# Kernel optimization log

Hardware: AMD Instinct MI355X
Metric: run time of the kernel (lower is better)

Reference implementation:

```python
import jax, jax.numpy as jnp
import numpy as np

B, T, A, C = 8, 256, 2, 128
R, H, OUT = 128, 128, 256  # readin_dim, session_embed_size, out_count


def _uni(k, shape, fan_in):
    # matches torch kaiming_uniform_(a=sqrt(5)) / nn.Linear default: U(-1/sqrt(fan_in), 1/sqrt(fan_in))
    b = 1.0 / np.sqrt(fan_in)
    return jax.random.uniform(k, shape, jnp.float32, -b, b)


def setup_inputs() -> dict:
    key = jax.random.key(0)
    ks = jax.random.split(key, 16)
    return {
        "state_in": jax.random.normal(ks[0], (B, T, A, C), jnp.float32),
        "session": jax.random.normal(ks[1], (B, H), jnp.float32),
        "subject": jax.random.normal(ks[2], (B, H), jnp.float32),
        "array": jax.random.normal(ks[3], (B, A, H), jnp.float32),
        "query": jax.random.normal(ks[4], (R,), jnp.float32),
        "pos_embeds": _uni(ks[5], (C, R), R),
        # key_project: Linear(R+H, R) -> GELU -> Linear(R, R); weights stored [in, out]
        "kW1": _uni(ks[6], (R + H, R), R + H), "kb1": _uni(ks[7], (R,), R + H),
        "kW2": _uni(ks[8], (R, R), R), "kb2": _uni(ks[9], (R,), R),
        # value_project: Linear(1+R+H, R) -> GELU -> Linear(R, OUT)
        # concat order in forward is [pos_embed (R), session (H), state_in (1)]
        "vW1": _uni(ks[10], (R + H + 1, R), R + H + 1), "vb1": _uni(ks[11], (R,), R + H + 1),
        "vW2": _uni(ks[12], (R, OUT), R), "vb2": _uni(ks[13], (OUT,), R),
    }


def reference(state_in, session, subject, array, query, pos_embeds,
              kW1, kb1, kW2, kb2, vW1, vb1, vW2, vb2):
    r = pos_embeds.shape[-1]
    h = session.shape[-1]
    scale = jnp.sqrt(jnp.asarray(r, state_in.dtype))
    # keys: cat([pos (c,r) expand b, session (b,h) expand c]) -> MLP. Decompose the
    # first Linear over the concat blocks (same math, no expanded concat buffer).
    kh = (pos_embeds @ kW1[:r])[None, :, :] + (session @ kW1[r:])[:, None, :] + kb1  # [b,c,r]
    keys = jax.nn.gelu(kh, approximate=False) @ kW2 + kb2                           # [b,c,r]
    # values: cat([pos, session, state_in]) over (b,t,a,c) -> MLP, decomposed likewise
    vh = ((pos_embeds @ vW1[:r])[None, None, None, :, :]
          + (session @ vW1[r:r + h])[:, None, None, None, :]
          + state_in[..., None] * vW1[r + h]
          + vb1)                                                                     # [b,t,a,c,r]
    values = jax.nn.gelu(vh, approximate=False) @ vW2 + vb2                          # [b,t,a,c,out]
    scores = jnp.einsum('bcr,r->bc', keys, query) / scale
    w = jax.nn.softmax(scores, axis=-1)                                              # [b,c]
    return jnp.einsum('bc,btach->btah', w, values)                                   # [b,t,a,out]
```

## Files before the change

### kernel.cpp

```cpp
#include <hip/hip_runtime.h>
#include <math.h>

#define B_ 8
#define T_ 256
#define A_ 2
#define C_ 128
#define R_ 128
#define H_ 128
#define OUT_ 256

#define WS_PCK 0
#define WS_PCV 16384
#define WS_PSK 32768
#define WS_PSV 33792
#define WS_QK  34816
#define WS_W   34944
#define WS_TOTAL 35968

__device__ __forceinline__ float gelu_fast(float x) {
    const float ax = fabsf(x);
    float q = fmaf(ax, 0.019527f, 0.000343654f);
    q = fmaf(q, ax, 0.1151945f);
    q = fmaf(q, ax, 0.19685217f);
    q = fmaf(q, ax, 1.0f);
    const float r  = __builtin_amdgcn_rcpf(q);
    const float r2 = r * r;
    const float r4 = r2 * r2;
    return fmaf(-0.5f * ax, r4, fmaxf(x, 0.0f));
}

__global__ __launch_bounds__(256) void prep_kernel(
    const float* __restrict__ session,
    const float* __restrict__ query,
    const float* __restrict__ pos,
    const float* __restrict__ kW1,
    const float* __restrict__ kb1,
    const float* __restrict__ kW2,
    const float* __restrict__ vW1,
    const float* __restrict__ vb1,
    float* __restrict__ ws)
{
    const int g = blockIdx.x * 256 + threadIdx.x;
    if (g < 16384) {
        const int c = g >> 7, r = g & 127;
        float acc = 0.0f;
        #pragma unroll 16
        for (int k = 0; k < R_; ++k)
            acc += pos[c * R_ + k] * kW1[k * R_ + r];
        ws[WS_PCK + g] = acc;
    } else if (g < 32768) {
        const int e = g - 16384;
        const int c = e >> 7, r = e & 127;
        float acc = 0.0f;
        #pragma unroll 16
        for (int k = 0; k < R_; ++k)
            acc += pos[c * R_ + k] * vW1[k * R_ + r];
        ws[WS_PCV + e] = acc;
    } else if (g < 33792) {
        const int e = g - 32768;
        const int b = e >> 7, r = e & 127;
        float acc = kb1[r];
        #pragma unroll 16
        for (int k = 0; k < H_; ++k)
            acc += session[b * H_ + k] * kW1[(R_ + k) * R_ + r];
        ws[WS_PSK + e] = acc;
    } else if (g < 34816) {
        const int e = g - 33792;
        const int b = e >> 7, r = e & 127;
        float acc = vb1[r];
        #pragma unroll 16
        for (int k = 0; k < H_; ++k)
            acc += session[b * H_ + k] * vW1[(R_ + k) * R_ + r];
        ws[WS_PSV + e] = acc;
    } else if (g < 34944) {
        const int r = g - 34816;
        float acc = 0.0f;
        #pragma unroll 16
        for (int j = 0; j < R_; ++j)
            acc += kW2[r * R_ + j] * query[j];
        ws[WS_QK + r] = acc;
    }
}

__global__ __launch_bounds__(512) void score_softmax_kernel(float* __restrict__ ws)
{
    __shared__ float pskL[R_];
    __shared__ float qkL[R_];
    __shared__ float part[4][C_];
    __shared__ float sc[C_];
    __shared__ float red[C_];

    const int b   = blockIdx.x;
    const int tid = threadIdx.x;
    const int q   = tid >> 7;
    const int c   = tid & 127;

    if (tid < 128) {
        pskL[tid] = ws[WS_PSK + b * R_ + tid];
        qkL[tid]  = ws[WS_QK + tid];
    }
    __syncthreads();

    const float* __restrict__ pckc = ws + WS_PCK + c * R_ + q * 32;
    float acc = 0.0f;
    #pragma unroll 8
    for (int i = 0; i < 32; ++i) {
        const float x = pckc[i] + pskL[q * 32 + i];
        acc += gelu_fast(x) * qkL[q * 32 + i];
    }
    part[q][c] = acc;
    __syncthreads();

    if (tid < 128) {
        const float s = (part[0][tid] + part[1][tid] + part[2][tid] + part[3][tid])
                        * 0.08838834764831845f;
        sc[tid]  = s;
        red[tid] = s;
    }
    __syncthreads();
    for (int st = 64; st > 0; st >>= 1) {
        if (tid < st) red[tid] = fmaxf(red[tid], red[tid + st]);
        __syncthreads();
    }
    const float m = red[0];
    __syncthreads();
    if (tid < 128) {
        const float e = __expf(sc[tid] - m);
        sc[tid]  = e;
        red[tid] = e;
    }
    __syncthreads();
    for (int st = 64; st > 0; st >>= 1) {
        if (tid < st) red[tid] += red[tid + st];
        __syncthreads();
    }
    if (tid < 128) ws[WS_W + b * C_ + tid] = sc[tid] / red[0];
}

__global__ __launch_bounds__(256) void main_kernel(
    const float* __restrict__ state,
    const float* __restrict__ vW1,
    const float* __restrict__ vW2,
    const float* __restrict__ vb2,
    const float* __restrict__ ws,
    float* __restrict__ out)
{
    __shared__ float4 p4[R_];

    const int blk  = blockIdx.x;
    const int b    = blk >> 7;
    const int grp  = blk & 127;
    const int tid  = threadIdx.x;
    const int r    = tid & 127;
    const int half = tid >> 7;

    const float* __restrict__ srow = state + (size_t)(b * 512 + grp * 4) * C_;
    const float* __restrict__ wb   = ws + WS_W + b * C_;

    const float vr    = vW1[(R_ + H_) * R_ + r];
    const float psv_r = ws[WS_PSV + b * R_ + r];

    float acc0 = 0.0f, acc1 = 0.0f, acc2 = 0.0f, acc3 = 0.0f;
    const int c0 = half * 64;
    const float* __restrict__ pcvr = ws + WS_PCV + r;
    #pragma unroll 8
    for (int c = c0; c < c0 + 64; ++c) {
        const float cc = pcvr[c * R_] + psv_r;
        const float wc = wb[c];
        const float s0 = srow[c];
        const float s1 = srow[C_ + c];
        const float s2 = srow[2 * C_ + c];
        const float s3 = srow[3 * C_ + c];
        acc0 = fmaf(wc, gelu_fast(fmaf(s0, vr, cc)), acc0);
        acc1 = fmaf(wc, gelu_fast(fmaf(s1, vr, cc)), acc1);
        acc2 = fmaf(wc, gelu_fast(fmaf(s2, vr, cc)), acc2);
        acc3 = fmaf(wc, gelu_fast(fmaf(s3, vr, cc)), acc3);
    }

    if (half == 0) p4[r] = make_float4(acc0, acc1, acc2, acc3);
    __syncthreads();
    if (half == 1) {
        float4 t = p4[r];
        t.x += acc0; t.y += acc1; t.z += acc2; t.w += acc3;
        p4[r] = t;
    }
    __syncthreads();

    const int h = tid;
    const float bias = vb2[h];
    float o0 = bias, o1 = bias, o2 = bias, o3 = bias;
    #pragma unroll 16
    for (int rr = 0; rr < R_; ++rr) {
        const float wcol = vW2[rr * OUT_ + h];
        const float4 pr = p4[rr];
        o0 = fmaf(pr.x, wcol, o0);
        o1 = fmaf(pr.y, wcol, o1);
        o2 = fmaf(pr.z, wcol, o2);
        o3 = fmaf(pr.w, wcol, o3);
    }
    float* __restrict__ orow = out + (size_t)(b * 512 + grp * 4) * OUT_;
    orow[0 * OUT_ + h] = o0;
    orow[1 * OUT_ + h] = o1;
    orow[2 * OUT_ + h] = o2;
    orow[3 * OUT_ + h] = o3;
}

extern "C" void kernel_launch(void* const* d_in, const int* in_sizes, int n_in,
                              void* d_out, int out_size, void* d_ws, size_t ws_size,
                              hipStream_t stream) {
    const float* state   = (const float*)d_in[0];
    const float* session = (const float*)d_in[1];
    const float* query   = (const float*)d_in[4];
    const float* pos     = (const float*)d_in[5];
    const float* kW1     = (const float*)d_in[6];
    const float* kb1     = (const float*)d_in[7];
    const float* kW2     = (const float*)d_in[8];
    const float* vW1     = (const float*)d_in[10];
    const float* vb1     = (const float*)d_in[11];
    const float* vW2     = (const float*)d_in[12];
    const float* vb2     = (const float*)d_in[13];

    float* ws  = (float*)d_ws;
    float* out = (float*)d_out;

    prep_kernel<<<137, 256, 0, stream>>>(session, query, pos, kW1, kb1, kW2,
                                         vW1, vb1, ws);
    score_softmax_kernel<<<B_, 512, 0, stream>>>(ws);
    main_kernel<<<B_ * 128, 256, 0, stream>>>(state, vW1, vW2, vb2, ws, out);
}
```

Before: 121.1 us.

## Stage state and weights in LDS and register-tile 4 r-columns per thread

```diff
diff --git a/kernel.cpp b/kernel.cpp
--- a/kernel.cpp
+++ b/kernel.cpp
@@ -145,44 +145,78 @@
     const float* __restrict__ ws,
     float* __restrict__ out)
 {
+    __shared__ __align__(16) float sv[4 * C_];
+    __shared__ float wv[C_];
+    __shared__ float4 part[8][R_];
     __shared__ float4 p4[R_];
 
-    const int blk  = blockIdx.x;
-    const int b    = blk >> 7;
-    const int grp  = blk & 127;
-    const int tid  = threadIdx.x;
-    const int r    = tid & 127;
-    const int half = tid >> 7;
-
+    const int blk = blockIdx.x;
+    const int b   = blk >> 7;
+    const int grp = blk & 127;
+    const int tid = threadIdx.x;
+    const int k   = tid & 31;
+    const int seg = tid >> 5;
+    const int r0  = k * 4;
+
+    if (tid < 128) wv[tid] = ws[WS_W + b * C_ + tid];
     const float* __restrict__ srow = state + (size_t)(b * 512 + grp * 4) * C_;
-    const float* __restrict__ wb   = ws + WS_W + b * C_;
-
-    const float vr    = vW1[(R_ + H_) * R_ + r];
-    const float psv_r = ws[WS_PSV + b * R_ + r];
-
-    float acc0 = 0.0f, acc1 = 0.0f, acc2 = 0.0f, acc3 = 0.0f;
-    const int c0 = half * 64;
-    const float* __restrict__ pcvr = ws + WS_PCV + r;
-    #pragma unroll 8
-    for (int c = c0; c < c0 + 64; ++c) {
-        const float cc = pcvr[c * R_] + psv_r;
-        const float wc = wb[c];
-        const float s0 = srow[c];
-        const float s1 = srow[C_ + c];
-        const float s2 = srow[2 * C_ + c];
-        const float s3 = srow[3 * C_ + c];
-        acc0 = fmaf(wc, gelu_fast(fmaf(s0, vr, cc)), acc0);
-        acc1 = fmaf(wc, gelu_fast(fmaf(s1, vr, cc)), acc1);
-        acc2 = fmaf(wc, gelu_fast(fmaf(s2, vr, cc)), acc2);
-        acc3 = fmaf(wc, gelu_fast(fmaf(s3, vr, cc)), acc3);
-    }
-
-    if (half == 0) p4[r] = make_float4(acc0, acc1, acc2, acc3);
-    __syncthreads();
-    if (half == 1) {
-        float4 t = p4[r];
-        t.x += acc0; t.y += acc1; t.z += acc2; t.w += acc3;
-        p4[r] = t;
+    sv[tid]       = srow[tid];
+    sv[tid + 256] = srow[tid + 256];
+
+    const float4 vr4  = *(const float4*)(vW1 + (R_ + H_) * R_ + r0);
+    const float4 psv4 = *(const float4*)(ws + WS_PSV + b * R_ + r0);
+    __syncthreads();
+
+    float4 a0 = make_float4(0.f, 0.f, 0.f, 0.f);
+    float4 a1 = a0, a2 = a0, a3 = a0;
+
+    const float* __restrict__ pcvb = ws + WS_PCV + r0;
+    const int cbeg = seg * 16;
+    #pragma unroll 2
+    for (int i = 0; i < 16; ++i) {
+        const int c = cbeg + i;
+        const float4 pv = *(const float4*)(pcvb + c * R_);
+        const float cc0 = pv.x + psv4.x;
+        const float cc1 = pv.y + psv4.y;
+        const float cc2 = pv.z + psv4.z;
+        const float cc3 = pv.w + psv4.w;
+        const float wc = wv[c];
+        const float s0 = sv[c];
+        const float s1 = sv[C_ + c];
+        const float s2 = sv[2 * C_ + c];
+        const float s3 = sv[3 * C_ + c];
+        a0.x = fmaf(wc, gelu_fast(fmaf(s0, vr4.x, cc0)), a0.x);
+        a0.y = fmaf(wc, gelu_fast(fmaf(s0, vr4.y, cc1)), a0.y);
+        a0.z = fmaf(wc, gelu_fast(fmaf(s0, vr4.z, cc2)), a0.z);
+        a0.w = fmaf(wc, gelu_fast(fmaf(s0, vr4.w, cc3)), a0.w);
+        a1.x = fmaf(wc, gelu_fast(fmaf(s1, vr4.x, cc0)), a1.x);
+        a1.y = fmaf(wc, gelu_fast(fmaf(s1, vr4.y, cc1)), a1.y);
+        a1.z = fmaf(wc, gelu_fast(fmaf(s1, vr4.z, cc2)), a1.z);
+        a1.w = fmaf(wc, gelu_fast(fmaf(s1, vr4.w, cc3)), a1.w);
+        a2.x = fmaf(wc, gelu_fast(fmaf(s2, vr4.x, cc0)), a2.x);
+        a2.y = fmaf(wc, gelu_fast(fmaf(s2, vr4.y, cc1)), a2.y);
+        a2.z = fmaf(wc, gelu_fast(fmaf(s2, vr4.z, cc2)), a2.z);
+        a2.w = fmaf(wc, gelu_fast(fmaf(s2, vr4.w, cc3)), a2.w);
+        a3.x = fmaf(wc, gelu_fast(fmaf(s3, vr4.x, cc0)), a3.x);
+        a3.y = fmaf(wc, gelu_fast(fmaf(s3, vr4.y, cc1)), a3.y);
+        a3.z = fmaf(wc, gelu_fast(fmaf(s3, vr4.z, cc2)), a3.z);
+        a3.w = fmaf(wc, gelu_fast(fmaf(s3, vr4.w, cc3)), a3.w);
+    }
+
+    part[seg][r0 + 0] = make_float4(a0.x, a1.x, a2.x, a3.x);
+    part[seg][r0 + 1] = make_float4(a0.y, a1.y, a2.y, a3.y);
+    part[seg][r0 + 2] = make_float4(a0.z, a1.z, a2.z, a3.z);
+    part[seg][r0 + 3] = make_float4(a0.w, a1.w, a2.w, a3.w);
+    __syncthreads();
+
+    if (tid < 128) {
+        float4 s = part[0][tid];
+        #pragma unroll
+        for (int sg = 1; sg < 8; ++sg) {
+            const float4 t = part[sg][tid];
+            s.x += t.x; s.y += t.y; s.z += t.z; s.w += t.w;
+        }
+        p4[tid] = s;
     }
     __syncthreads();
 
```

Result: faster. 117.5 us (-3.0%).
